# Kernel tuning notes

Measured on AMD Instinct MI355X. Metric: run time of the kernel, lower is better.

The kernel has to match this reference:

```python
import jax, jax.numpy as jnp
import numpy as np

N_NODES = 100000
N_EDGES = 1600000
DIM = 128


def setup_inputs() -> dict:
    key = jax.random.key(0)
    k1, k2, k3, k4, k5 = jax.random.split(key, 5)
    x = jax.random.normal(k1, (N_NODES, DIM), dtype=jnp.float32)
    edge_index = jax.random.randint(k2, (2, N_EDGES), 0, N_NODES, dtype=jnp.int64)
    s = 1.0 / np.sqrt(DIM)
    W_lin = jax.random.uniform(k3, (DIM, DIM), jnp.float32, -s, s)   # nn.Linear (bias=False)
    W_gcn = jax.random.uniform(k4, (DIM, DIM), jnp.float32, -s, s)   # GCNConv internal lin (bias=False)
    b_gcn = jax.random.uniform(k5, (DIM,), jnp.float32, -s, s)       # GCNConv bias
    return {"x": x, "edge_index": edge_index, "W_lin": W_lin, "W_gcn": W_gcn, "b_gcn": b_gcn}


def reference(x, edge_index, W_lin, W_gcn, b_gcn):
    N = x.shape[0]
    # self.linear (bias=False) then GCNConv's internal linear (bias=False)
    h = (x @ W_lin.T) @ W_gcn.T                                      # [N, D]
    # add self loops (PyG GCNConv default add_self_loops=True)
    loop = jnp.arange(N, dtype=edge_index.dtype)
    row = jnp.concatenate([edge_index[0], loop])                     # source
    col = jnp.concatenate([edge_index[1], loop])                     # target
    # symmetric normalization: deg over targets incl. self loops
    deg = jax.ops.segment_sum(jnp.ones_like(col, dtype=h.dtype), col, num_segments=N)
    dinv = jnp.where(deg > 0, jax.lax.rsqrt(deg), 0.0)               # deg^{-1/2}, inf->0
    norm = dinv[row] * dinv[col]                                     # [E+N]
    # gather -> scale -> scatter-add (aggr='add', flow source_to_target)
    msg = h[row] * norm[:, None]                                     # [E+N, D]
    out = jax.ops.segment_sum(msg, col, num_segments=N) + b_gcn      # [N, D]
    # NOTE: self.relu is `Sequential as ReLU` -> empty Sequential -> identity
    return out
```

## Files before the change

kernel.cpp:

```cpp
#include <hip/hip_runtime.h>
#include <hip/hip_bf16.h>

#define DIM 128
#define NBUCK 2048
#define BCAP 1344

typedef short bf16x8 __attribute__((ext_vector_type(8)));
typedef float f32x4 __attribute__((ext_vector_type(4)));

__device__ __forceinline__ unsigned short f2bf(float f) {
    __hip_bfloat16 h = __float2bfloat16(f);
    return *reinterpret_cast<unsigned short*>(&h);
}
__device__ __forceinline__ float u2f(unsigned int u) {
    union { unsigned int i; float f; } v; v.i = u; return v.f;
}
__device__ __forceinline__ unsigned int f2u(float f) {
    union { float f; unsigned int i; } v; v.f = f; return v.i;
}

__global__ __launch_bounds__(128) void wp_kernel(const float* __restrict__ Wg,
                                                 const float* __restrict__ Wl,
                                                 unsigned short* __restrict__ Wpb,
                                                 int* __restrict__ bcur) {
    const int c = blockIdx.x;
    const int k = threadIdx.x;
    const int gid = c * 128 + k;
    if (gid < NBUCK) bcur[gid] = 0;
    float s = 0.f;
    for (int j = 0; j < DIM; ++j)
        s = fmaf(Wg[c * DIM + j], Wl[j * DIM + k], s);
    Wpb[c * DIM + k] = f2bf(s);
}

__global__ __launch_bounds__(256) void part_gemm_kernel(
        const int* __restrict__ src, const int* __restrict__ dst,
        int* __restrict__ bcur, unsigned int* __restrict__ ebuf,
        int E, int nchunk,
        const float* __restrict__ x, const unsigned short* __restrict__ Wpb,
        unsigned int* __restrict__ hbu, int N) {
    __shared__ __align__(16) char smem[49152];
    const int t = threadIdx.x;

    if (blockIdx.x < 256) {
        int* hist = (int*)smem;
        int* base = hist + NBUCK;
        for (int i = t; i < NBUCK; i += 256) hist[i] = 0;
        __syncthreads();

        const int e0 = blockIdx.x * nchunk;
        const int e1 = min(e0 + nchunk, E);
        for (int e = e0 + t; e < e1; e += 256)
            atomicAdd(&hist[dst[e] >> 6], 1);
        __syncthreads();

        for (int i = t; i < NBUCK; i += 256) {
            const int cc = hist[i];
            base[i] = (cc > 0) ? atomicAdd(&bcur[i], cc) : 0;
        }
        __syncthreads();

        for (int e = e0 + t; e < e1; e += 256) {
            const int d = dst[e];
            const int b = d >> 6;
            const int pos = atomicAdd(&base[b], 1);
            if (pos < BCAP) {
                const unsigned int p = (unsigned int)src[e] | ((unsigned int)(d & 63) << 17);
                ebuf[(size_t)b * BCAP + pos] = p;
            }
        }
        return;
    }

    unsigned short* xs  = (unsigned short*)smem;
    unsigned short* wps = xs + 64 * 128;
    const int brow = (blockIdx.x - 256) * 64;

#pragma unroll
    for (int j = 0; j < 8; ++j) {
        const int col = (t >> 4) + j * 16;
        const int kb = t & 15;
        const uint4 v = *(const uint4*)(Wpb + col * 128 + kb * 8);
        *(uint4*)&wps[col * 128 + ((kb ^ (col & 15)) * 8)] = v;
    }
#pragma unroll
    for (int i = 0; i < 4; ++i) {
        const int row = (t >> 4) + i * 16;
        const int kb = t & 15;
        const int g = brow + row;
        float4 a0 = make_float4(0.f, 0.f, 0.f, 0.f), a1 = a0;
        if (g < N) {
            a0 = *(const float4*)(x + (size_t)g * 128 + kb * 8);
            a1 = *(const float4*)(x + (size_t)g * 128 + kb * 8 + 4);
        }
        ushort4 lo, hi;
        lo.x = f2bf(a0.x); lo.y = f2bf(a0.y); lo.z = f2bf(a0.z); lo.w = f2bf(a0.w);
        hi.x = f2bf(a1.x); hi.y = f2bf(a1.y); hi.z = f2bf(a1.z); hi.w = f2bf(a1.w);
        unsigned short* p = &xs[row * 128 + ((kb ^ (row & 15)) * 8)];
        *(ushort4*)p = lo;
        *(ushort4*)(p + 4) = hi;
    }
    __syncthreads();

    const int lane = t & 63, wv = t >> 6;
    const int m16 = lane & 15, quad = lane >> 4;

    f32x4 acc[8];
#pragma unroll
    for (int ct = 0; ct < 8; ++ct) acc[ct] = (f32x4){0.f, 0.f, 0.f, 0.f};

    const int arow = wv * 16 + m16;
#pragma unroll
    for (int s = 0; s < 4; ++s) {
        const int pk = ((s * 4 + quad) ^ m16) * 8;
        const bf16x8 a = *(const bf16x8*)&xs[arow * 128 + pk];
#pragma unroll
        for (int ct = 0; ct < 8; ++ct) {
            const bf16x8 b = *(const bf16x8*)&wps[(ct * 16 + m16) * 128 + pk];
            acc[ct] = __builtin_amdgcn_mfma_f32_16x16x32_bf16(a, b, acc[ct], 0, 0, 0);
        }
    }

    const int r0 = brow + wv * 16 + quad * 4;
#pragma unroll
    for (int ct = 0; ct < 4; ++ct) {
        const int col = ct * 16 + m16;
#pragma unroll
        for (int r = 0; r < 4; ++r) {
            if (r0 + r < N) {
                const unsigned int pk = (unsigned int)f2bf(acc[ct][r]) |
                                        ((unsigned int)f2bf(acc[ct + 4][r]) << 16);
                hbu[(size_t)(r0 + r) * 64 + col] = pk;
            }
        }
    }
}

__global__ __launch_bounds__(256) void bcount_kernel(const unsigned int* __restrict__ ebuf,
                                                     const int* __restrict__ bcur,
                                                     int* __restrict__ degi,
                                                     float* __restrict__ dinv, int N) {
    __shared__ int cnt[64];
    const int t = threadIdx.x;
    const int bkt = blockIdx.x;
    if (t < 64) cnt[t] = 0;
    __syncthreads();
    const int c = min(bcur[bkt], BCAP);
    const unsigned int* eb = ebuf + (size_t)bkt * BCAP;
    for (int i = t; i < c; i += 256)
        atomicAdd(&cnt[eb[i] >> 17], 1);
    __syncthreads();
    if (t < 64) {
        const int node = (bkt << 6) + t;
        if (node < N) {
            degi[node] = cnt[t];
            dinv[node] = rsqrtf((float)(cnt[t] + 1));
        }
    }
}

__global__ __launch_bounds__(256) void sortgather_kernel(
        const unsigned int* __restrict__ hbu, const unsigned int* __restrict__ ebuf,
        const int* __restrict__ bcur, const int* __restrict__ degi,
        const float* __restrict__ dinv,
        const float* __restrict__ b, float* __restrict__ out, int N) {
    __shared__ unsigned int pairs[BCAP * 2];
    __shared__ int cnt[64];
    __shared__ int scn[64];
    __shared__ int st[64];
    __shared__ int deg[64];
    const int t   = threadIdx.x;
    const int bkt = blockIdx.x;
    const int c   = min(bcur[bkt], BCAP);
    const unsigned int* eb = ebuf + (size_t)bkt * BCAP;
    const int n0 = bkt << 6;

    if (t < 64) {
        const int node = n0 + t;
        const int d = (node < N) ? degi[node] : 0;
        deg[t] = d;
        scn[t] = d;
    }
    __syncthreads();
    for (int off = 1; off < 64; off <<= 1) {
        int v = (t < 64 && t >= off) ? scn[t - off] : 0;
        __syncthreads();
        if (t < 64) scn[t] += v;
        __syncthreads();
    }
    if (t < 64) {
        const int excl = scn[t] - deg[t];
        st[t]  = excl;
        cnt[t] = excl;
    }
    __syncthreads();

    for (int i = t; i < c; i += 256) {
        const unsigned int p = eb[i];
        const int s = (int)(p & 0x1FFFF);
        const int pos = atomicAdd(&cnt[p >> 17], 1);
        uint2 pr; pr.x = (unsigned int)s; pr.y = f2u(dinv[s]);
        *(uint2*)&pairs[2 * pos] = pr;
    }
    __syncthreads();

    const int lane = t & 63;
    const int wv   = t >> 6;
    const float bx = b[lane];
    const float by = b[lane + 64];

    for (int i = 0; i < 16; ++i) {
        const int dl = wv * 16 + i;
        const int node = n0 + dl;
        if (node >= N) continue;
        const int dgi = deg[dl];
        const float dv = rsqrtf((float)(dgi + 1));
        const unsigned int self = hbu[(size_t)node * 64 + lane];
        float ax = dv * u2f(self << 16);
        float ay = dv * u2f(self & 0xFFFF0000u);

        const int jb = st[dl];
        const int je = jb + dgi;
        int j = jb;
        for (; j + 8 <= je; j += 8) {
            const uint2 p0 = *(const uint2*)&pairs[2 * (j + 0)];
            const uint2 p1 = *(const uint2*)&pairs[2 * (j + 1)];
            const uint2 p2 = *(const uint2*)&pairs[2 * (j + 2)];
            const uint2 p3 = *(const uint2*)&pairs[2 * (j + 3)];
            const uint2 p4 = *(const uint2*)&pairs[2 * (j + 4)];
            const uint2 p5 = *(const uint2*)&pairs[2 * (j + 5)];
            const uint2 p6 = *(const uint2*)&pairs[2 * (j + 6)];
            const uint2 p7 = *(const uint2*)&pairs[2 * (j + 7)];
            const unsigned int v0 = hbu[(size_t)p0.x * 64 + lane];
            const unsigned int v1 = hbu[(size_t)p1.x * 64 + lane];
            const unsigned int v2 = hbu[(size_t)p2.x * 64 + lane];
            const unsigned int v3 = hbu[(size_t)p3.x * 64 + lane];
            const unsigned int v4 = hbu[(size_t)p4.x * 64 + lane];
            const unsigned int v5 = hbu[(size_t)p5.x * 64 + lane];
            const unsigned int v6 = hbu[(size_t)p6.x * 64 + lane];
            const unsigned int v7 = hbu[(size_t)p7.x * 64 + lane];
            ax = fmaf(u2f(v0 << 16), u2f(p0.y), ax);
            ax = fmaf(u2f(v1 << 16), u2f(p1.y), ax);
            ax = fmaf(u2f(v2 << 16), u2f(p2.y), ax);
            ax = fmaf(u2f(v3 << 16), u2f(p3.y), ax);
            ax = fmaf(u2f(v4 << 16), u2f(p4.y), ax);
            ax = fmaf(u2f(v5 << 16), u2f(p5.y), ax);
            ax = fmaf(u2f(v6 << 16), u2f(p6.y), ax);
            ax = fmaf(u2f(v7 << 16), u2f(p7.y), ax);
            ay = fmaf(u2f(v0 & 0xFFFF0000u), u2f(p0.y), ay);
            ay = fmaf(u2f(v1 & 0xFFFF0000u), u2f(p1.y), ay);
            ay = fmaf(u2f(v2 & 0xFFFF0000u), u2f(p2.y), ay);
            ay = fmaf(u2f(v3 & 0xFFFF0000u), u2f(p3.y), ay);
            ay = fmaf(u2f(v4 & 0xFFFF0000u), u2f(p4.y), ay);
            ay = fmaf(u2f(v5 & 0xFFFF0000u), u2f(p5.y), ay);
            ay = fmaf(u2f(v6 & 0xFFFF0000u), u2f(p6.y), ay);
            ay = fmaf(u2f(v7 & 0xFFFF0000u), u2f(p7.y), ay);
        }
        for (; j + 2 <= je; j += 2) {
            const uint2 p0 = *(const uint2*)&pairs[2 * (j + 0)];
            const uint2 p1 = *(const uint2*)&pairs[2 * (j + 1)];
            const unsigned int v0 = hbu[(size_t)p0.x * 64 + lane];
            const unsigned int v1 = hbu[(size_t)p1.x * 64 + lane];
            ax = fmaf(u2f(v0 << 16), u2f(p0.y), ax);
            ax = fmaf(u2f(v1 << 16), u2f(p1.y), ax);
            ay = fmaf(u2f(v0 & 0xFFFF0000u), u2f(p0.y), ay);
            ay = fmaf(u2f(v1 & 0xFFFF0000u), u2f(p1.y), ay);
        }
        for (; j < je; ++j) {
            const uint2 pr = *(const uint2*)&pairs[2 * j];
            const unsigned int v = hbu[(size_t)pr.x * 64 + lane];
            ax = fmaf(u2f(v << 16), u2f(pr.y), ax);
            ay = fmaf(u2f(v & 0xFFFF0000u), u2f(pr.y), ay);
        }
        out[(size_t)node * 128 + lane]      = dv * ax + bx;
        out[(size_t)node * 128 + 64 + lane] = dv * ay + by;
    }
}

extern "C" void kernel_launch(void* const* d_in, const int* in_sizes, int n_in,
                              void* d_out, int out_size, void* d_ws, size_t ws_size,
                              hipStream_t stream) {
    const float* x  = (const float*)d_in[0];
    const int*   ei = (const int*)d_in[1];
    const float* Wl = (const float*)d_in[2];
    const float* Wg = (const float*)d_in[3];
    const float* bg = (const float*)d_in[4];

    const int N = in_sizes[0] / DIM;
    const int E = in_sizes[1] / 2;
    const int* srcIdx = ei;
    const int* dstIdx = ei + E;

    char* wsb = (char*)d_ws;
    unsigned short* Wpb  = (unsigned short*)(wsb + 0);
    int*            bcur = (int*)(wsb + 65536);
    int*            degi = (int*)(wsb + 131072);
    float*          dinv = (float*)(wsb + 589824);
    unsigned int*   ebuf = (unsigned int*)(wsb + 2097152);
    unsigned int*   hbu  = (unsigned int*)(wsb + 16777216);
    const size_t needed = 16777216ull + (size_t)N * DIM * 2;
    if (ws_size < needed) return;

    const int nbkt = (N + 63) >> 6;
    const int ngemm = (N + 63) / 64;
    const int nchunk = (E + 255) / 256;

    wp_kernel        <<<DIM, DIM, 0, stream>>>(Wg, Wl, Wpb, bcur);
    part_gemm_kernel <<<256 + ngemm, 256, 0, stream>>>(srcIdx, dstIdx, bcur, ebuf,
                                                       E, nchunk, x, Wpb, hbu, N);
    bcount_kernel    <<<nbkt, 256, 0, stream>>>(ebuf, bcur, degi, dinv, N);
    sortgather_kernel<<<nbkt, 256, 0, stream>>>(hbu, ebuf, bcur, degi, dinv, bg,
                                                (float*)d_out, N);
}
```

Measured before the change: 221.2 us.

## Fuse all stages into one persistent cooperative kernel with grid syncs

Replaces the four separate launches (weight product, partition+GEMM, degree count, sort-gather) with a single cooperative persistent kernel that uses grid-wide syncs between phases and grid-stride loops over buckets and tiles. The GEMM now reads the pre-swizzled weight matrix directly from global/L2 instead of staging it in shared memory, which shrinks shared memory to allow more resident blocks. This is meant to remove launch overhead and inter-kernel gaps. In exchange the weight product is spread over the whole grid with a serial inner loop, the grid syncs add cost, and the GEMM issues uncached-in-LDS weight loads. Fewer blocks are resident for the gather phase than the original one-block-per-bucket launch.

```diff
diff --git a/kernel.cpp b/kernel.cpp
--- a/kernel.cpp
+++ b/kernel.cpp
@@ -1,9 +1,13 @@
 #include <hip/hip_runtime.h>
 #include <hip/hip_bf16.h>
+#include <hip/hip_cooperative_groups.h>
+
+namespace cg = cooperative_groups;
 
 #define DIM 128
 #define NBUCK 2048
 #define BCAP 1344
+#define NPART 256
 
 typedef short bf16x8 __attribute__((ext_vector_type(8)));
 typedef float f32x4 __attribute__((ext_vector_type(4)));
@@ -19,261 +23,242 @@
     union { float f; unsigned int i; } v; v.f = f; return v.i;
 }
 
-__global__ __launch_bounds__(128) void wp_kernel(const float* __restrict__ Wg,
-                                                 const float* __restrict__ Wl,
-                                                 unsigned short* __restrict__ Wpb,
-                                                 int* __restrict__ bcur) {
-    const int c = blockIdx.x;
-    const int k = threadIdx.x;
-    const int gid = c * 128 + k;
-    if (gid < NBUCK) bcur[gid] = 0;
-    float s = 0.f;
-    for (int j = 0; j < DIM; ++j)
-        s = fmaf(Wg[c * DIM + j], Wl[j * DIM + k], s);
-    Wpb[c * DIM + k] = f2bf(s);
-}
-
-__global__ __launch_bounds__(256) void part_gemm_kernel(
-        const int* __restrict__ src, const int* __restrict__ dst,
-        int* __restrict__ bcur, unsigned int* __restrict__ ebuf,
-        int E, int nchunk,
-        const float* __restrict__ x, const unsigned short* __restrict__ Wpb,
-        unsigned int* __restrict__ hbu, int N) {
-    __shared__ __align__(16) char smem[49152];
-    const int t = threadIdx.x;
-
-    if (blockIdx.x < 256) {
+__global__ __launch_bounds__(256, 6) void fused_kernel(
+        const float* __restrict__ x, const int* __restrict__ src,
+        const int* __restrict__ dst, const float* __restrict__ Wg,
+        const float* __restrict__ Wl, const float* __restrict__ bg,
+        unsigned short* __restrict__ Wps, int* __restrict__ bcur,
+        int* __restrict__ degi, float* __restrict__ dinv,
+        unsigned int* __restrict__ ebuf, unsigned int* __restrict__ hbu,
+        float* __restrict__ out,
+        int N, int E, int nchunk, int nbkt, int ntile) {
+    __shared__ __align__(16) char smem[16384];
+    const int t   = threadIdx.x;
+    const int bid = blockIdx.x;
+    const int G   = gridDim.x;
+    cg::grid_group gg = cg::this_grid();
+
+    for (int id = bid * 256 + t; id < DIM * DIM; id += G * 256) {
+        const int col = id >> 7, k = id & 127;
+        float s = 0.f;
+        for (int j = 0; j < DIM; ++j)
+            s = fmaf(Wg[col * DIM + j], Wl[j * DIM + k], s);
+        Wps[col * 128 + (((k >> 3) ^ (col & 15)) << 3) + (k & 7)] = f2bf(s);
+    }
+    for (int id = bid * 256 + t; id < NBUCK; id += G * 256) bcur[id] = 0;
+    gg.sync();
+
+    if (bid < NPART) {
         int* hist = (int*)smem;
         int* base = hist + NBUCK;
         for (int i = t; i < NBUCK; i += 256) hist[i] = 0;
         __syncthreads();
-
-        const int e0 = blockIdx.x * nchunk;
+        const int e0 = bid * nchunk;
         const int e1 = min(e0 + nchunk, E);
         for (int e = e0 + t; e < e1; e += 256)
             atomicAdd(&hist[dst[e] >> 6], 1);
         __syncthreads();
-
         for (int i = t; i < NBUCK; i += 256) {
             const int cc = hist[i];
             base[i] = (cc > 0) ? atomicAdd(&bcur[i], cc) : 0;
         }
         __syncthreads();
-
         for (int e = e0 + t; e < e1; e += 256) {
             const int d = dst[e];
             const int b = d >> 6;
             const int pos = atomicAdd(&base[b], 1);
-            if (pos < BCAP) {
-                const unsigned int p = (unsigned int)src[e] | ((unsigned int)(d & 63) << 17);
-                ebuf[(size_t)b * BCAP + pos] = p;
-            }
-        }
-        return;
+            if (pos < BCAP)
+                ebuf[(size_t)b * BCAP + pos] =
+                    (unsigned int)src[e] | ((unsigned int)(d & 63) << 17);
+        }
+    } else {
+        unsigned short* xs = (unsigned short*)smem;
+        const int lane = t & 63, wv = t >> 6;
+        const int m16 = lane & 15, quad = lane >> 4;
+        for (int tile = bid - NPART; tile < ntile; tile += G - NPART) {
+            const int brow = tile * 64;
+#pragma unroll
+            for (int i = 0; i < 4; ++i) {
+                const int row = (t >> 4) + i * 16;
+                const int kb = t & 15;
+                const int g = brow + row;
+                float4 a0 = make_float4(0.f, 0.f, 0.f, 0.f), a1 = a0;
+                if (g < N) {
+                    a0 = *(const float4*)(x + (size_t)g * 128 + kb * 8);
+                    a1 = *(const float4*)(x + (size_t)g * 128 + kb * 8 + 4);
+                }
+                ushort4 lo, hi;
+                lo.x = f2bf(a0.x); lo.y = f2bf(a0.y); lo.z = f2bf(a0.z); lo.w = f2bf(a0.w);
+                hi.x = f2bf(a1.x); hi.y = f2bf(a1.y); hi.z = f2bf(a1.z); hi.w = f2bf(a1.w);
+                unsigned short* p = &xs[row * 128 + ((kb ^ (row & 15)) * 8)];
+                *(ushort4*)p = lo;
+                *(ushort4*)(p + 4) = hi;
+            }
+            __syncthreads();
+
+            f32x4 acc[8];
+#pragma unroll
+            for (int ct = 0; ct < 8; ++ct) acc[ct] = (f32x4){0.f, 0.f, 0.f, 0.f};
+
+            const int arow = wv * 16 + m16;
+            int pk[4];
+            bf16x8 afrag[4];
+#pragma unroll
+            for (int s = 0; s < 4; ++s) {
+                pk[s] = ((s * 4 + quad) ^ m16) * 8;
+                afrag[s] = *(const bf16x8*)&xs[arow * 128 + pk[s]];
+            }
+#pragma unroll
+            for (int ct = 0; ct < 8; ++ct) {
+#pragma unroll
+                for (int s = 0; s < 4; ++s) {
+                    const bf16x8 b = *(const bf16x8*)&Wps[(ct * 16 + m16) * 128 + pk[s]];
+                    acc[ct] = __builtin_amdgcn_mfma_f32_16x16x32_bf16(afrag[s], b, acc[ct], 0, 0, 0);
+                }
+            }
+
+            const int r0 = brow + wv * 16 + quad * 4;
+#pragma unroll
+            for (int ct = 0; ct < 4; ++ct) {
+                const int col = ct * 16 + m16;
+#pragma unroll
+                for (int r = 0; r < 4; ++r) {
+                    if (r0 + r < N) {
+                        const unsigned int pkd = (unsigned int)f2bf(acc[ct][r]) |
+                                                 ((unsigned int)f2bf(acc[ct + 4][r]) << 16);
+                        hbu[(size_t)(r0 + r) * 64 + col] = pkd;
+                    }
+                }
+            }
+            __syncthreads();
+        }
     }
-
-    unsigned short* xs  = (unsigned short*)smem;
-    unsigned short* wps = xs + 64 * 128;
-    const int brow = (blockIdx.x - 256) * 64;
-
-#pragma unroll
-    for (int j = 0; j < 8; ++j) {
-        const int col = (t >> 4) + j * 16;
-        const int kb = t & 15;
-        const uint4 v = *(const uint4*)(Wpb + col * 128 + kb * 8);
-        *(uint4*)&wps[col * 128 + ((kb ^ (col & 15)) * 8)] = v;
+    gg.sync();
+
+    {
+        int* cnt = (int*)smem;
+        for (int bkt = bid; bkt < nbkt; bkt += G) {
+            if (t < 64) cnt[t] = 0;
+            __syncthreads();
+            const int c = min(bcur[bkt], BCAP);
+            const unsigned int* eb = ebuf + (size_t)bkt * BCAP;
+            for (int i = t; i < c; i += 256)
+                atomicAdd(&cnt[eb[i] >> 17], 1);
+            __syncthreads();
+            if (t < 64) {
+                const int node = (bkt << 6) + t;
+                if (node < N) {
+                    degi[node] = cnt[t];
+                    dinv[node] = rsqrtf((float)(cnt[t] + 1));
+                }
+            }
+            __syncthreads();
+        }
     }
-#pragma unroll
-    for (int i = 0; i < 4; ++i) {
-        const int row = (t >> 4) + i * 16;
-        const int kb = t & 15;
-        const int g = brow + row;
-        float4 a0 = make_float4(0.f, 0.f, 0.f, 0.f), a1 = a0;
-        if (g < N) {
-            a0 = *(const float4*)(x + (size_t)g * 128 + kb * 8);
-            a1 = *(const float4*)(x + (size_t)g * 128 + kb * 8 + 4);
-        }
-        ushort4 lo, hi;
-        lo.x = f2bf(a0.x); lo.y = f2bf(a0.y); lo.z = f2bf(a0.z); lo.w = f2bf(a0.w);
-        hi.x = f2bf(a1.x); hi.y = f2bf(a1.y); hi.z = f2bf(a1.z); hi.w = f2bf(a1.w);
-        unsigned short* p = &xs[row * 128 + ((kb ^ (row & 15)) * 8)];
-        *(ushort4*)p = lo;
-        *(ushort4*)(p + 4) = hi;
-    }
-    __syncthreads();
-
-    const int lane = t & 63, wv = t >> 6;
-    const int m16 = lane & 15, quad = lane >> 4;
-
-    f32x4 acc[8];
-#pragma unroll
-    for (int ct = 0; ct < 8; ++ct) acc[ct] = (f32x4){0.f, 0.f, 0.f, 0.f};
-
-    const int arow = wv * 16 + m16;
-#pragma unroll
-    for (int s = 0; s < 4; ++s) {
-        const int pk = ((s * 4 + quad) ^ m16) * 8;
-        const bf16x8 a = *(const bf16x8*)&xs[arow * 128 + pk];
-#pragma unroll
-        for (int ct = 0; ct < 8; ++ct) {
-            const bf16x8 b = *(const bf16x8*)&wps[(ct * 16 + m16) * 128 + pk];
-            acc[ct] = __builtin_amdgcn_mfma_f32_16x16x32_bf16(a, b, acc[ct], 0, 0, 0);
-        }
-    }
-
-    const int r0 = brow + wv * 16 + quad * 4;
-#pragma unroll
-    for (int ct = 0; ct < 4; ++ct) {
-        const int col = ct * 16 + m16;
-#pragma unroll
-        for (int r = 0; r < 4; ++r) {
-            if (r0 + r < N) {
-                const unsigned int pk = (unsigned int)f2bf(acc[ct][r]) |
-                                        ((unsigned int)f2bf(acc[ct + 4][r]) << 16);
-                hbu[(size_t)(r0 + r) * 64 + col] = pk;
-            }
-        }
-    }
-}
-
-__global__ __launch_bounds__(256) void bcount_kernel(const unsigned int* __restrict__ ebuf,
-                                                     const int* __restrict__ bcur,
-                                                     int* __restrict__ degi,
-                                                     float* __restrict__ dinv, int N) {
-    __shared__ int cnt[64];
-    const int t = threadIdx.x;
-    const int bkt = blockIdx.x;
-    if (t < 64) cnt[t] = 0;
-    __syncthreads();
-    const int c = min(bcur[bkt], BCAP);
-    const unsigned int* eb = ebuf + (size_t)bkt * BCAP;
-    for (int i = t; i < c; i += 256)
-        atomicAdd(&cnt[eb[i] >> 17], 1);
-    __syncthreads();
-    if (t < 64) {
-        const int node = (bkt << 6) + t;
-        if (node < N) {
-            degi[node] = cnt[t];
-            dinv[node] = rsqrtf((float)(cnt[t] + 1));
-        }
-    }
-}
-
-__global__ __launch_bounds__(256) void sortgather_kernel(
-        const unsigned int* __restrict__ hbu, const unsigned int* __restrict__ ebuf,
-        const int* __restrict__ bcur, const int* __restrict__ degi,
-        const float* __restrict__ dinv,
-        const float* __restrict__ b, float* __restrict__ out, int N) {
-    __shared__ unsigned int pairs[BCAP * 2];
-    __shared__ int cnt[64];
-    __shared__ int scn[64];
-    __shared__ int st[64];
-    __shared__ int deg[64];
-    const int t   = threadIdx.x;
-    const int bkt = blockIdx.x;
-    const int c   = min(bcur[bkt], BCAP);
-    const unsigned int* eb = ebuf + (size_t)bkt * BCAP;
-    const int n0 = bkt << 6;
-
-    if (t < 64) {
-        const int node = n0 + t;
-        const int d = (node < N) ? degi[node] : 0;
-        deg[t] = d;
-        scn[t] = d;
-    }
-    __syncthreads();
-    for (int off = 1; off < 64; off <<= 1) {
-        int v = (t < 64 && t >= off) ? scn[t - off] : 0;
-        __syncthreads();
-        if (t < 64) scn[t] += v;
-        __syncthreads();
-    }
-    if (t < 64) {
-        const int excl = scn[t] - deg[t];
-        st[t]  = excl;
-        cnt[t] = excl;
-    }
-    __syncthreads();
-
-    for (int i = t; i < c; i += 256) {
-        const unsigned int p = eb[i];
-        const int s = (int)(p & 0x1FFFF);
-        const int pos = atomicAdd(&cnt[p >> 17], 1);
-        uint2 pr; pr.x = (unsigned int)s; pr.y = f2u(dinv[s]);
-        *(uint2*)&pairs[2 * pos] = pr;
-    }
-    __syncthreads();
-
-    const int lane = t & 63;
-    const int wv   = t >> 6;
-    const float bx = b[lane];
-    const float by = b[lane + 64];
-
-    for (int i = 0; i < 16; ++i) {
-        const int dl = wv * 16 + i;
-        const int node = n0 + dl;
-        if (node >= N) continue;
-        const int dgi = deg[dl];
-        const float dv = rsqrtf((float)(dgi + 1));
-        const unsigned int self = hbu[(size_t)node * 64 + lane];
-        float ax = dv * u2f(self << 16);
-        float ay = dv * u2f(self & 0xFFFF0000u);
-
-        const int jb = st[dl];
-        const int je = jb + dgi;
-        int j = jb;
-        for (; j + 8 <= je; j += 8) {
-            const uint2 p0 = *(const uint2*)&pairs[2 * (j + 0)];
-            const uint2 p1 = *(const uint2*)&pairs[2 * (j + 1)];
-            const uint2 p2 = *(const uint2*)&pairs[2 * (j + 2)];
-            const uint2 p3 = *(const uint2*)&pairs[2 * (j + 3)];
-            const uint2 p4 = *(const uint2*)&pairs[2 * (j + 4)];
-            const uint2 p5 = *(const uint2*)&pairs[2 * (j + 5)];
-            const uint2 p6 = *(const uint2*)&pairs[2 * (j + 6)];
-            const uint2 p7 = *(const uint2*)&pairs[2 * (j + 7)];
-            const unsigned int v0 = hbu[(size_t)p0.x * 64 + lane];
-            const unsigned int v1 = hbu[(size_t)p1.x * 64 + lane];
-            const unsigned int v2 = hbu[(size_t)p2.x * 64 + lane];
-            const unsigned int v3 = hbu[(size_t)p3.x * 64 + lane];
-            const unsigned int v4 = hbu[(size_t)p4.x * 64 + lane];
-            const unsigned int v5 = hbu[(size_t)p5.x * 64 + lane];
-            const unsigned int v6 = hbu[(size_t)p6.x * 64 + lane];
-            const unsigned int v7 = hbu[(size_t)p7.x * 64 + lane];
-            ax = fmaf(u2f(v0 << 16), u2f(p0.y), ax);
-            ax = fmaf(u2f(v1 << 16), u2f(p1.y), ax);
-            ax = fmaf(u2f(v2 << 16), u2f(p2.y), ax);
-            ax = fmaf(u2f(v3 << 16), u2f(p3.y), ax);
-            ax = fmaf(u2f(v4 << 16), u2f(p4.y), ax);
-            ax = fmaf(u2f(v5 << 16), u2f(p5.y), ax);
-            ax = fmaf(u2f(v6 << 16), u2f(p6.y), ax);
-            ax = fmaf(u2f(v7 << 16), u2f(p7.y), ax);
-            ay = fmaf(u2f(v0 & 0xFFFF0000u), u2f(p0.y), ay);
-            ay = fmaf(u2f(v1 & 0xFFFF0000u), u2f(p1.y), ay);
-            ay = fmaf(u2f(v2 & 0xFFFF0000u), u2f(p2.y), ay);
-            ay = fmaf(u2f(v3 & 0xFFFF0000u), u2f(p3.y), ay);
-            ay = fmaf(u2f(v4 & 0xFFFF0000u), u2f(p4.y), ay);
-            ay = fmaf(u2f(v5 & 0xFFFF0000u), u2f(p5.y), ay);
-            ay = fmaf(u2f(v6 & 0xFFFF0000u), u2f(p6.y), ay);
-            ay = fmaf(u2f(v7 & 0xFFFF0000u), u2f(p7.y), ay);
-        }
-        for (; j + 2 <= je; j += 2) {
-            const uint2 p0 = *(const uint2*)&pairs[2 * (j + 0)];
-            const uint2 p1 = *(const uint2*)&pairs[2 * (j + 1)];
-            const unsigned int v0 = hbu[(size_t)p0.x * 64 + lane];
-            const unsigned int v1 = hbu[(size_t)p1.x * 64 + lane];
-            ax = fmaf(u2f(v0 << 16), u2f(p0.y), ax);
-            ax = fmaf(u2f(v1 << 16), u2f(p1.y), ax);
-            ay = fmaf(u2f(v0 & 0xFFFF0000u), u2f(p0.y), ay);
-            ay = fmaf(u2f(v1 & 0xFFFF0000u), u2f(p1.y), ay);
-        }
-        for (; j < je; ++j) {
-            const uint2 pr = *(const uint2*)&pairs[2 * j];
-            const unsigned int v = hbu[(size_t)pr.x * 64 + lane];
-            ax = fmaf(u2f(v << 16), u2f(pr.y), ax);
-            ay = fmaf(u2f(v & 0xFFFF0000u), u2f(pr.y), ay);
-        }
-        out[(size_t)node * 128 + lane]      = dv * ax + bx;
-        out[(size_t)node * 128 + 64 + lane] = dv * ay + by;
+    gg.sync();
+
+    {
+        unsigned int* pairs = (unsigned int*)smem;
+        int* cnt = (int*)(smem + 10752);
+        int* scn = cnt + 64;
+        int* st  = scn + 64;
+        int* deg = st + 64;
+        const int lane = t & 63, wv = t >> 6;
+        const float bx = bg[lane];
+        const float by = bg[lane + 64];
+
+        for (int bkt = bid; bkt < nbkt; bkt += G) {
+            const int n0 = bkt << 6;
+            const int c = min(bcur[bkt], BCAP);
+            const unsigned int* eb = ebuf + (size_t)bkt * BCAP;
+
+            if (t < 64) {
+                const int node = n0 + t;
+                const int d = (node < N) ? degi[node] : 0;
+                deg[t] = d;
+                scn[t] = d;
+            }
+            __syncthreads();
+            for (int off = 1; off < 64; off <<= 1) {
+                int v = (t < 64 && t >= off) ? scn[t - off] : 0;
+                __syncthreads();
+                if (t < 64) scn[t] += v;
+                __syncthreads();
+            }
+            if (t < 64) {
+                const int excl = scn[t] - deg[t];
+                st[t]  = excl;
+                cnt[t] = excl;
+            }
+            __syncthreads();
+
+            for (int i = t; i < c; i += 256) {
+                const unsigned int p = eb[i];
+                const int s = (int)(p & 0x1FFFF);
+                const int pos = atomicAdd(&cnt[p >> 17], 1);
+                uint2 pr; pr.x = (unsigned int)s; pr.y = f2u(dinv[s]);
+                *(uint2*)&pairs[2 * pos] = pr;
+            }
+            __syncthreads();
+
+            for (int i = 0; i < 16; ++i) {
+                const int dl = wv * 16 + i;
+                const int node = n0 + dl;
+                if (node >= N) continue;
+                const int dgi = deg[dl];
+                const float dv = rsqrtf((float)(dgi + 1));
+                const unsigned int self = hbu[(size_t)node * 64 + lane];
+                float ax = dv * u2f(self << 16);
+                float ay = dv * u2f(self & 0xFFFF0000u);
+
+                const int jb = st[dl];
+                const int je = jb + dgi;
+                int j = jb;
+                for (; j + 8 <= je; j += 8) {
+                    const uint2 p0 = *(const uint2*)&pairs[2 * (j + 0)];
+                    const uint2 p1 = *(const uint2*)&pairs[2 * (j + 1)];
+                    const uint2 p2 = *(const uint2*)&pairs[2 * (j + 2)];
+                    const uint2 p3 = *(const uint2*)&pairs[2 * (j + 3)];
+                    const uint2 p4 = *(const uint2*)&pairs[2 * (j + 4)];
+                    const uint2 p5 = *(const uint2*)&pairs[2 * (j + 5)];
+                    const uint2 p6 = *(const uint2*)&pairs[2 * (j + 6)];
+                    const uint2 p7 = *(const uint2*)&pairs[2 * (j + 7)];
+                    const unsigned int v0 = hbu[(size_t)p0.x * 64 + lane];
+                    const unsigned int v1 = hbu[(size_t)p1.x * 64 + lane];
+                    const unsigned int v2 = hbu[(size_t)p2.x * 64 + lane];
+                    const unsigned int v3 = hbu[(size_t)p3.x * 64 + lane];
+                    const unsigned int v4 = hbu[(size_t)p4.x * 64 + lane];
+                    const unsigned int v5 = hbu[(size_t)p5.x * 64 + lane];
+                    const unsigned int v6 = hbu[(size_t)p6.x * 64 + lane];
+                    const unsigned int v7 = hbu[(size_t)p7.x * 64 + lane];
+                    ax = fmaf(u2f(v0 << 16), u2f(p0.y), ax);
+                    ax = fmaf(u2f(v1 << 16), u2f(p1.y), ax);
+                    ax = fmaf(u2f(v2 << 16), u2f(p2.y), ax);
+                    ax = fmaf(u2f(v3 << 16), u2f(p3.y), ax);
+                    ax = fmaf(u2f(v4 << 16), u2f(p4.y), ax);
+                    ax = fmaf(u2f(v5 << 16), u2f(p5.y), ax);
+                    ax = fmaf(u2f(v6 << 16), u2f(p6.y), ax);
+                    ax = fmaf(u2f(v7 << 16), u2f(p7.y), ax);
+                    ay = fmaf(u2f(v0 & 0xFFFF0000u), u2f(p0.y), ay);
+                    ay = fmaf(u2f(v1 & 0xFFFF0000u), u2f(p1.y), ay);
+                    ay = fmaf(u2f(v2 & 0xFFFF0000u), u2f(p2.y), ay);
+                    ay = fmaf(u2f(v3 & 0xFFFF0000u), u2f(p3.y), ay);
+                    ay = fmaf(u2f(v4 & 0xFFFF0000u), u2f(p4.y), ay);
+                    ay = fmaf(u2f(v5 & 0xFFFF0000u), u2f(p5.y), ay);
+                    ay = fmaf(u2f(v6 & 0xFFFF0000u), u2f(p6.y), ay);
+                    ay = fmaf(u2f(v7 & 0xFFFF0000u), u2f(p7.y), ay);
+                }
+                for (; j < je; ++j) {
+                    const uint2 pr = *(const uint2*)&pairs[2 * j];
+                    const unsigned int v = hbu[(size_t)pr.x * 64 + lane];
+                    ax = fmaf(u2f(v << 16), u2f(pr.y), ax);
+                    ay = fmaf(u2f(v & 0xFFFF0000u), u2f(pr.y), ay);
+                }
+                out[(size_t)node * 128 + lane]      = dv * ax + bx;
+                out[(size_t)node * 128 + 64 + lane] = dv * ay + by;
+            }
+            __syncthreads();
+        }
     }
 }
 
@@ -292,7 +277,7 @@
     const int* dstIdx = ei + E;
 
     char* wsb = (char*)d_ws;
-    unsigned short* Wpb  = (unsigned short*)(wsb + 0);
+    unsigned short* Wps  = (unsigned short*)(wsb + 0);
     int*            bcur = (int*)(wsb + 65536);
     int*            degi = (int*)(wsb + 131072);
     float*          dinv = (float*)(wsb + 589824);
@@ -301,14 +286,26 @@
     const size_t needed = 16777216ull + (size_t)N * DIM * 2;
     if (ws_size < needed) return;
 
-    const int nbkt = (N + 63) >> 6;
-    const int ngemm = (N + 63) / 64;
-    const int nchunk = (E + 255) / 256;
-
-    wp_kernel        <<<DIM, DIM, 0, stream>>>(Wg, Wl, Wpb, bcur);
-    part_gemm_kernel <<<256 + ngemm, 256, 0, stream>>>(srcIdx, dstIdx, bcur, ebuf,
-                                                       E, nchunk, x, Wpb, hbu, N);
-    bcount_kernel    <<<nbkt, 256, 0, stream>>>(ebuf, bcur, degi, dinv, N);
-    sortgather_kernel<<<nbkt, 256, 0, stream>>>(hbu, ebuf, bcur, degi, dinv, bg,
-                                                (float*)d_out, N);
-}
+    const int nbkt  = (N + 63) >> 6;
+    const int ntile = (N + 63) >> 6;
+    const int nchunk = (E + NPART - 1) / NPART;
+
+    int nb = 0;
+    if (hipOccupancyMaxActiveBlocksPerMultiprocessor(&nb, fused_kernel, 256, 0)
+            != hipSuccess || nb < 2) nb = 2;
+    if (nb > 8) nb = 8;
+    int grid = nb * 256;
+    if (grid > 2048) grid = 2048;
+
+    const float* xp = x; const int* sp = srcIdx; const int* dp = dstIdx;
+    const float* wgp = Wg; const float* wlp = Wl; const float* bgp = bg;
+    unsigned short* wpsp = Wps; int* bcurp = bcur; int* degip = degi;
+    float* dinvp = dinv; unsigned int* ebufp = ebuf; unsigned int* hbup = hbu;
+    float* outp = (float*)d_out;
+    int Nv = N, Ev = E, nchunkv = nchunk, nbktv = nbkt, ntilev = ntile;
+
+    void* args[] = { &xp, &sp, &dp, &wgp, &wlp, &bgp, &wpsp, &bcurp, &degip,
+                     &dinvp, &ebufp, &hbup, &outp, &Nv, &Ev, &nchunkv, &nbktv, &ntilev };
+    hipLaunchCooperativeKernel((const void*)fused_kernel, dim3(grid), dim3(256),
+                               args, 0, stream);
+}
```

Result: slower. 551.1 us (+149.1%).

## Regroup kernels: fuse weight product with partition, GEMM with bucket count

Applied to the files above, without the earlier changes.

The small weight-product kernel is folded into the edge-partition launch as extra blocks, and the bucket-degree counting is folded into the GEMM launch as extra blocks. The bucket-counter zeroing moves to a hipMemsetAsync. The work per stage is unchanged, but there is one fewer kernel launch and the tiny serial weight-product launch no longer sits alone on the critical path. The cost is that the partition step can no longer overlap the GEMM, since the GEMM now needs Wpb from the earlier launch, and the memset adds a separate operation.

```diff
diff --git a/kernel.cpp b/kernel.cpp
--- a/kernel.cpp
+++ b/kernel.cpp
@@ -4,6 +4,7 @@
 #define DIM 128
 #define NBUCK 2048
 #define BCAP 1344
+#define NPART 256
 
 typedef short bf16x8 __attribute__((ext_vector_type(8)));
 typedef float f32x4 __attribute__((ext_vector_type(4)));
@@ -19,54 +20,75 @@
     union { float f; unsigned int i; } v; v.f = f; return v.i;
 }
 
-__global__ __launch_bounds__(128) void wp_kernel(const float* __restrict__ Wg,
-                                                 const float* __restrict__ Wl,
-                                                 unsigned short* __restrict__ Wpb,
-                                                 int* __restrict__ bcur) {
-    const int c = blockIdx.x;
-    const int k = threadIdx.x;
-    const int gid = c * 128 + k;
-    if (gid < NBUCK) bcur[gid] = 0;
-    float s = 0.f;
-    for (int j = 0; j < DIM; ++j)
-        s = fmaf(Wg[c * DIM + j], Wl[j * DIM + k], s);
-    Wpb[c * DIM + k] = f2bf(s);
-}
-
-__global__ __launch_bounds__(256) void part_gemm_kernel(
+__global__ __launch_bounds__(256) void part_wp_kernel(
         const int* __restrict__ src, const int* __restrict__ dst,
         int* __restrict__ bcur, unsigned int* __restrict__ ebuf,
         int E, int nchunk,
+        const float* __restrict__ Wg, const float* __restrict__ Wl,
+        unsigned short* __restrict__ Wpb) {
+    __shared__ int hist[NBUCK];
+    __shared__ int base[NBUCK];
+    const int t = threadIdx.x;
+
+    if (blockIdx.x >= NPART) {
+        const int id = (blockIdx.x - NPART) * 256 + t;
+        const int c = id >> 7, k = id & 127;
+        float s = 0.f;
+        for (int j = 0; j < DIM; ++j)
+            s = fmaf(Wg[c * DIM + j], Wl[j * DIM + k], s);
+        Wpb[c * DIM + k] = f2bf(s);
+        return;
+    }
+
+    for (int i = t; i < NBUCK; i += 256) hist[i] = 0;
+    __syncthreads();
+
+    const int e0 = blockIdx.x * nchunk;
+    const int e1 = min(e0 + nchunk, E);
+    for (int e = e0 + t; e < e1; e += 256)
+        atomicAdd(&hist[dst[e] >> 6], 1);
+    __syncthreads();
+
+    for (int i = t; i < NBUCK; i += 256) {
+        const int cc = hist[i];
+        base[i] = (cc > 0) ? atomicAdd(&bcur[i], cc) : 0;
+    }
+    __syncthreads();
+
+    for (int e = e0 + t; e < e1; e += 256) {
+        const int d = dst[e];
+        const int b = d >> 6;
+        const int pos = atomicAdd(&base[b], 1);
+        if (pos < BCAP)
+            ebuf[(size_t)b * BCAP + pos] =
+                (unsigned int)src[e] | ((unsigned int)(d & 63) << 17);
+    }
+}
+
+__global__ __launch_bounds__(256) void gemm_bcount_kernel(
         const float* __restrict__ x, const unsigned short* __restrict__ Wpb,
-        unsigned int* __restrict__ hbu, int N) {
+        unsigned int* __restrict__ hbu,
+        const unsigned int* __restrict__ ebuf, const int* __restrict__ bcur,
+        int* __restrict__ degi, float* __restrict__ dinv,
+        int N, int ntile) {
     __shared__ __align__(16) char smem[49152];
     const int t = threadIdx.x;
 
-    if (blockIdx.x < 256) {
-        int* hist = (int*)smem;
-        int* base = hist + NBUCK;
-        for (int i = t; i < NBUCK; i += 256) hist[i] = 0;
+    if (blockIdx.x >= ntile) {
+        int* cnt = (int*)smem;
+        const int bkt = blockIdx.x - ntile;
+        if (t < 64) cnt[t] = 0;
         __syncthreads();
-
-        const int e0 = blockIdx.x * nchunk;
-        const int e1 = min(e0 + nchunk, E);
-        for (int e = e0 + t; e < e1; e += 256)
-            atomicAdd(&hist[dst[e] >> 6], 1);
+        const int c = min(bcur[bkt], BCAP);
+        const unsigned int* eb = ebuf + (size_t)bkt * BCAP;
+        for (int i = t; i < c; i += 256)
+            atomicAdd(&cnt[eb[i] >> 17], 1);
         __syncthreads();
-
-        for (int i = t; i < NBUCK; i += 256) {
-            const int cc = hist[i];
-            base[i] = (cc > 0) ? atomicAdd(&bcur[i], cc) : 0;
-        }
-        __syncthreads();
-
-        for (int e = e0 + t; e < e1; e += 256) {
-            const int d = dst[e];
-            const int b = d >> 6;
-            const int pos = atomicAdd(&base[b], 1);
-            if (pos < BCAP) {
-                const unsigned int p = (unsigned int)src[e] | ((unsigned int)(d & 63) << 17);
-                ebuf[(size_t)b * BCAP + pos] = p;
+        if (t < 64) {
+            const int node = (bkt << 6) + t;
+            if (node < N) {
+                degi[node] = cnt[t];
+                dinv[node] = rsqrtf((float)(cnt[t] + 1));
             }
         }
         return;
@@ -74,7 +96,7 @@
 
     unsigned short* xs  = (unsigned short*)smem;
     unsigned short* wps = xs + 64 * 128;
-    const int brow = (blockIdx.x - 256) * 64;
+    const int brow = blockIdx.x * 64;
 
 #pragma unroll
     for (int j = 0; j < 8; ++j) {
@@ -132,29 +154,6 @@
                                         ((unsigned int)f2bf(acc[ct + 4][r]) << 16);
                 hbu[(size_t)(r0 + r) * 64 + col] = pk;
             }
-        }
-    }
-}
-
-__global__ __launch_bounds__(256) void bcount_kernel(const unsigned int* __restrict__ ebuf,
-                                                     const int* __restrict__ bcur,
-                                                     int* __restrict__ degi,
-                                                     float* __restrict__ dinv, int N) {
-    __shared__ int cnt[64];
-    const int t = threadIdx.x;
-    const int bkt = blockIdx.x;
-    if (t < 64) cnt[t] = 0;
-    __syncthreads();
-    const int c = min(bcur[bkt], BCAP);
-    const unsigned int* eb = ebuf + (size_t)bkt * BCAP;
-    for (int i = t; i < c; i += 256)
-        atomicAdd(&cnt[eb[i] >> 17], 1);
-    __syncthreads();
-    if (t < 64) {
-        const int node = (bkt << 6) + t;
-        if (node < N) {
-            degi[node] = cnt[t];
-            dinv[node] = rsqrtf((float)(cnt[t] + 1));
         }
     }
 }
@@ -301,14 +300,15 @@
     const size_t needed = 16777216ull + (size_t)N * DIM * 2;
     if (ws_size < needed) return;
 
-    const int nbkt = (N + 63) >> 6;
-    const int ngemm = (N + 63) / 64;
-    const int nchunk = (E + 255) / 256;
-
-    wp_kernel        <<<DIM, DIM, 0, stream>>>(Wg, Wl, Wpb, bcur);
-    part_gemm_kernel <<<256 + ngemm, 256, 0, stream>>>(srcIdx, dstIdx, bcur, ebuf,
-                                                       E, nchunk, x, Wpb, hbu, N);
-    bcount_kernel    <<<nbkt, 256, 0, stream>>>(ebuf, bcur, degi, dinv, N);
-    sortgather_kernel<<<nbkt, 256, 0, stream>>>(hbu, ebuf, bcur, degi, dinv, bg,
-                                                (float*)d_out, N);
-}
+    const int nbkt  = (N + 63) >> 6;
+    const int ntile = (N + 63) >> 6;
+    const int nchunk = (E + NPART - 1) / NPART;
+
+    hipMemsetAsync(bcur, 0, NBUCK * sizeof(int), stream);
+    part_wp_kernel    <<<NPART + 64, 256, 0, stream>>>(srcIdx, dstIdx, bcur, ebuf,
+                                                       E, nchunk, Wg, Wl, Wpb);
+    gemm_bcount_kernel<<<ntile + nbkt, 256, 0, stream>>>(x, Wpb, hbu, ebuf, bcur,
+                                                         degi, dinv, N, ntile);
+    sortgather_kernel <<<nbkt, 256, 0, stream>>>(hbu, ebuf, bcur, degi, dinv, bg,
+                                                 (float*)d_out, N);
+}
```

New measurement: 218.5 us. Within noise of the previous version (-1.2%).
